# Optimization experiments

Measured on AMD Instinct MI355X. Metric: run time of the kernel, lower is better.

The kernel has to match this reference:

```python
import jax, jax.numpy as jnp
import numpy as np
from jax import lax


def setup_inputs() -> dict:
    key = jax.random.key(0)
    k1, k2 = jax.random.split(key)
    C, H, W = 64, 224, 224
    C_out, hf, wf = 128, 3, 3
    x = jax.random.normal(k1, (C, H, W), dtype=jnp.float32)
    kernels = jax.random.normal(k2, (C_out, C, hf, wf), dtype=jnp.float32)
    return {"x": x, "kernels": kernels}


def reference(x, kernels):
    # Original builds im2col columns per output pixel then does k_col @ x_col,
    # i.e. a cross-correlation with 'valid' padding and stride 1.
    # lax.conv_general_dilated computes exactly this (no kernel flip).
    stride = 1
    out = lax.conv_general_dilated(
        x[None],                       # (1, C, H, W) NCHW
        kernels,                       # (C_out, C_in, hf, wf) OIHW
        window_strides=(stride, stride),
        padding="VALID",
        dimension_numbers=("NCHW", "OIHW", "NCHW"),
    )
    return out[0]                      # (C_out, H_out, W_out)
```

## Files before the change

kernel.cpp:

```cpp
#include <hip/hip_runtime.h>
#include <hip/hip_bf16.h>


#define H_IN   224
#define W_IN   224
#define C_OUT  128
#define H_OUT  222
#define W_OUT  222
#define XP     226
#define CPAD   72
#define TW     68

#define PREP_W_UNITS 288
#define PREP_UNITS   1192

typedef __attribute__((ext_vector_type(8)))  short bf16x8;
typedef __attribute__((ext_vector_type(16))) float f32x16;

static __device__ __forceinline__ unsigned short f2bs(float f) {
    union { __hip_bfloat16 h; unsigned short u; } cv;
    cv.h = __float2bfloat16(f);
    return cv.u;
}

__global__ __launch_bounds__(256)
void prep_kernel(const float* __restrict__ x, const float* __restrict__ w,
                 __hip_bfloat16* __restrict__ xt, __hip_bfloat16* __restrict__ wt)
{
    __shared__ __align__(16) unsigned short tile[64 * TW];
    const int u = blockIdx.x;
    const int t = threadIdx.x;

    if (u < PREP_W_UNITS) {
        int idx = u * 256 + t;
        int ij  = idx >> 13;
        int rem = idx & 8191;
        int co  = rem >> 6;
        int c   = rem & 63;
        wt[((ij * 8 + (c >> 3)) * 128 + co) * 8 + (c & 7)] =
            __float2bfloat16(w[(co * 64 + c) * 9 + ij]);
        return;
    }

    const int ux = u - PREP_W_UNITS;
    const int h  = ux >> 2;
    const int w0 = (ux & 3) * 64;

    {
        const int wq = (t & 15) * 4;
        const int c0 = t >> 4;
        #pragma unroll
        for (int p = 0; p < 4; ++p) {
            const int c  = c0 + p * 16;
            const int wg = w0 + wq;
            float4 v = make_float4(0.f, 0.f, 0.f, 0.f);
            if (h < H_IN && wg < W_IN)
                v = *(const float4*)(x + ((size_t)c * H_IN + h) * W_IN + wg);
            ushort4 b;
            b.x = f2bs(v.x); b.y = f2bs(v.y); b.z = f2bs(v.z); b.w = f2bs(v.w);
            *(ushort4*)(tile + c * TW + wq) = b;
        }
    }
    __syncthreads();

    {
        const int wl = t >> 2;
        const int cq = (t & 3) * 16;
        const int wg = w0 + wl;
        if (wg < XP) {
            alignas(16) unsigned short r[16];
            #pragma unroll
            for (int k = 0; k < 16; ++k)
                r[k] = tile[(cq + k) * TW + wl];
            float4* d = (float4*)((unsigned short*)xt + ((size_t)h * XP + wg) * 64 + cq);
            d[0] = ((const float4*)r)[0];
            d[1] = ((const float4*)r)[1];
        }
    }
}

__global__ __launch_bounds__(128, 2)
void conv_mfma_kernel(const __hip_bfloat16* __restrict__ xt,
                      const __hip_bfloat16* __restrict__ wt,
                      float* __restrict__ out)
{
    __shared__ __hip_bfloat16 xs[6 * 34 * CPAD];
    const int ow0 = blockIdx.x * 32;
    const int oh0 = blockIdx.y * 4;
    const int co0 = blockIdx.z * 64;
    const int tid = threadIdx.x;

    for (int q = tid; q < 6 * 34 * 8; q += 128) {
        int sub = q & 7;
        int pix = q >> 3;
        int row = pix / 34;
        int wc  = pix - row * 34;
        *(float4*)(xs + (row * 34 + wc) * CPAD + sub * 8) =
            *(const float4*)(xt + ((oh0 + row) * XP + (ow0 + wc)) * 64 + sub * 8);
    }
    __syncthreads();

    const int wave = tid >> 6;
    const int lane = tid & 63;
    const int n    = lane & 31;
    const int h    = lane >> 5;
    const int r0   = wave * 2;

    f32x16 acc[2][2] = {};

    #pragma unroll
    for (int p = 0; p < 9; ++p) {
        const int i  = p / 3;
        const int jj = p - i * 3;
        #pragma unroll
        for (int t = 0; t < 4; ++t) {
            bf16x8 afr[2], bfr[2];
            #pragma unroll
            for (int mi = 0; mi < 2; ++mi)
                afr[mi] = *(const bf16x8*)(wt +
                    (size_t)(((p * 8 + t * 2 + h) * 128 + co0 + mi * 32 + n) * 8));
            #pragma unroll
            for (int ni = 0; ni < 2; ++ni)
                bfr[ni] = *(const bf16x8*)(xs +
                    ((i + r0 + ni) * 34 + n + jj) * CPAD + t * 16 + h * 8);
            #pragma unroll
            for (int mi = 0; mi < 2; ++mi)
                #pragma unroll
                for (int ni = 0; ni < 2; ++ni)
                    acc[mi][ni] = __builtin_amdgcn_mfma_f32_32x32x16_bf16(
                        afr[mi], bfr[ni], acc[mi][ni], 0, 0, 0);
        }
    }

    #pragma unroll
    for (int mi = 0; mi < 2; ++mi) {
        #pragma unroll
        for (int ni = 0; ni < 2; ++ni) {
            const int oh = oh0 + r0 + ni;
            const int ow = ow0 + n;
            if (oh < H_OUT && ow < W_OUT) {
                #pragma unroll
                for (int r = 0; r < 16; ++r) {
                    int co = co0 + mi * 32 + (r & 3) + 8 * (r >> 2) + 4 * h;
                    out[(size_t)co * (H_OUT * W_OUT) + oh * W_OUT + ow] = acc[mi][ni][r];
                }
            }
        }
    }
}

extern "C" void kernel_launch(void* const* d_in, const int* in_sizes, int n_in,
                              void* d_out, int out_size, void* d_ws, size_t ws_size,
                              hipStream_t stream)
{
    const float* x = (const float*)d_in[0];
    const float* w = (const float*)d_in[1];
    float* out     = (float*)d_out;

    __hip_bfloat16* xt = (__hip_bfloat16*)d_ws;
    __hip_bfloat16* wt = (__hip_bfloat16*)((char*)d_ws + (size_t)XP * XP * 64 * 2);

    prep_kernel<<<PREP_UNITS, 256, 0, stream>>>(x, w, xt, wt);
    conv_mfma_kernel<<<dim3(7, 56, 2), 128, 0, stream>>>(xt, wt, out);
}
```

Measured before the change: 88.39 us.

## Fuse input bf16 conversion and transpose into conv kernel's shared-memory load

Removes the separate input transpose pass that wrote a channel-last bf16 copy of the input to workspace. The conv kernel now reads fp32 input directly, converts each element to bf16 and packs 8 channels per shared-memory store. The prep kernel is reduced to converting weights only. This saves a global round trip and part of a launch. In exchange, each conv block issues strided per-channel scalar loads of fp32 data, including halo overlap between blocks.

```diff
diff --git a/kernel.cpp b/kernel.cpp
--- a/kernel.cpp
+++ b/kernel.cpp
@@ -7,12 +7,7 @@
 #define C_OUT  128
 #define H_OUT  222
 #define W_OUT  222
-#define XP     226
 #define CPAD   72
-#define TW     68
-
-#define PREP_W_UNITS 288
-#define PREP_UNITS   1192
 
 typedef __attribute__((ext_vector_type(8)))  short bf16x8;
 typedef __attribute__((ext_vector_type(16))) float f32x16;
@@ -24,63 +19,21 @@
 }
 
 __global__ __launch_bounds__(256)
-void prep_kernel(const float* __restrict__ x, const float* __restrict__ w,
-                 __hip_bfloat16* __restrict__ xt, __hip_bfloat16* __restrict__ wt)
+void transform_w_kernel(const float* __restrict__ w, __hip_bfloat16* __restrict__ wt)
 {
-    __shared__ __align__(16) unsigned short tile[64 * TW];
-    const int u = blockIdx.x;
-    const int t = threadIdx.x;
-
-    if (u < PREP_W_UNITS) {
-        int idx = u * 256 + t;
+    int idx = blockIdx.x * 256 + threadIdx.x;
+    if (idx < 9 * 128 * 64) {
         int ij  = idx >> 13;
         int rem = idx & 8191;
         int co  = rem >> 6;
         int c   = rem & 63;
         wt[((ij * 8 + (c >> 3)) * 128 + co) * 8 + (c & 7)] =
             __float2bfloat16(w[(co * 64 + c) * 9 + ij]);
-        return;
-    }
-
-    const int ux = u - PREP_W_UNITS;
-    const int h  = ux >> 2;
-    const int w0 = (ux & 3) * 64;
-
-    {
-        const int wq = (t & 15) * 4;
-        const int c0 = t >> 4;
-        #pragma unroll
-        for (int p = 0; p < 4; ++p) {
-            const int c  = c0 + p * 16;
-            const int wg = w0 + wq;
-            float4 v = make_float4(0.f, 0.f, 0.f, 0.f);
-            if (h < H_IN && wg < W_IN)
-                v = *(const float4*)(x + ((size_t)c * H_IN + h) * W_IN + wg);
-            ushort4 b;
-            b.x = f2bs(v.x); b.y = f2bs(v.y); b.z = f2bs(v.z); b.w = f2bs(v.w);
-            *(ushort4*)(tile + c * TW + wq) = b;
-        }
-    }
-    __syncthreads();
-
-    {
-        const int wl = t >> 2;
-        const int cq = (t & 3) * 16;
-        const int wg = w0 + wl;
-        if (wg < XP) {
-            alignas(16) unsigned short r[16];
-            #pragma unroll
-            for (int k = 0; k < 16; ++k)
-                r[k] = tile[(cq + k) * TW + wl];
-            float4* d = (float4*)((unsigned short*)xt + ((size_t)h * XP + wg) * 64 + cq);
-            d[0] = ((const float4*)r)[0];
-            d[1] = ((const float4*)r)[1];
-        }
     }
 }
 
 __global__ __launch_bounds__(128, 2)
-void conv_mfma_kernel(const __hip_bfloat16* __restrict__ xt,
+void conv_mfma_kernel(const float* __restrict__ x,
                       const __hip_bfloat16* __restrict__ wt,
                       float* __restrict__ out)
 {
@@ -90,13 +43,24 @@
     const int co0 = blockIdx.z * 64;
     const int tid = threadIdx.x;
 
-    for (int q = tid; q < 6 * 34 * 8; q += 128) {
-        int sub = q & 7;
-        int pix = q >> 3;
-        int row = pix / 34;
-        int wc  = pix - row * 34;
-        *(float4*)(xs + (row * 34 + wc) * CPAD + sub * 8) =
-            *(const float4*)(xt + ((oh0 + row) * XP + (ow0 + wc)) * 64 + sub * 8);
+    for (int q = tid; q < 6 * 8 * 34; q += 128) {
+        const int wc  = q % 34;
+        const int rs  = q / 34;
+        const int row = rs >> 3;
+        const int sub = rs & 7;
+        const int hh  = oh0 + row;
+        const int ww  = ow0 + wc;
+        alignas(16) unsigned short r[8];
+        if (hh < H_IN && ww < W_IN) {
+            const float* src = x + ((size_t)(sub * 8) * H_IN + hh) * W_IN + ww;
+            #pragma unroll
+            for (int j = 0; j < 8; ++j)
+                r[j] = f2bs(src[(size_t)j * H_IN * W_IN]);
+        } else {
+            #pragma unroll
+            for (int j = 0; j < 8; ++j) r[j] = 0;
+        }
+        *(float4*)(xs + (row * 34 + wc) * CPAD + sub * 8) = *(const float4*)r;
     }
     __syncthreads();
 
@@ -157,9 +121,8 @@
     const float* w = (const float*)d_in[1];
     float* out     = (float*)d_out;
 
-    __hip_bfloat16* xt = (__hip_bfloat16*)d_ws;
-    __hip_bfloat16* wt = (__hip_bfloat16*)((char*)d_ws + (size_t)XP * XP * 64 * 2);
+    __hip_bfloat16* wt = (__hip_bfloat16*)d_ws;
 
-    prep_kernel<<<PREP_UNITS, 256, 0, stream>>>(x, w, xt, wt);
-    conv_mfma_kernel<<<dim3(7, 56, 2), 128, 0, stream>>>(xt, wt, out);
+    transform_w_kernel<<<288, 256, 0, stream>>>(w, wt);
+    conv_mfma_kernel<<<dim3(7, 56, 2), 128, 0, stream>>>(x, wt, out);
 }
```

Measured after the change: 88.44 us. About the same (+0.1%).
